# Kernel optimization log

Measured on AMD Instinct MI355X. Metric: run time of the kernel, lower is better.

## Reference

```python
import jax, jax.numpy as jnp
import numpy as np

N_TOKENS = 16384   # flat tokens (e.g., 16 images x 1024 tokens)
E_DIM = 2048       # codebook_dim
N_E = 16384        # codebook_size


def setup_inputs() -> dict:
    key = jax.random.key(0)
    kx, ke = jax.random.split(key)
    x = jax.random.normal(kx, (N_TOKENS, E_DIM), dtype=jnp.float32)
    # nn.Embedding init: uniform(-1/n_e, 1/n_e); scale a normal sample similarly for a realistic magnitude
    embedding = jax.random.uniform(ke, (N_E, E_DIM), dtype=jnp.float32,
                                   minval=-1.0 / N_E, maxval=1.0 / N_E)
    return {"x": x, "embedding": embedding}


def reference(x, embedding):
    # IBQ.quantize, inference path (is_train=False):
    # d[b, n] = ||x_b||^2 + ||e_n||^2 - 2 <x_b, e_n>
    d = (jnp.sum(x * x, axis=1, keepdims=True)
         + jnp.sum(embedding * embedding, axis=1)
         - 2.0 * jnp.einsum('bd,nd->bn', x, embedding))  # [B, n_e]
    min_encoding_indices = jnp.argmin(d, axis=1)          # [B]
    z_q = embedding[min_encoding_indices]                 # [B, e_dim]
    # VQ.forward returns (x, code_idx, codebook_loss=None); loss omitted (non-tensor None)
    return (z_q, min_encoding_indices)
```

## Files before the change

### kernel.cpp

```cpp
#include <hip/hip_runtime.h>
#include <stdint.h>
#include <float.h>

#define K_DIM 2048
#define M_TOK 16384
#define N_EMB 16384
#define NKT 32

typedef int i32x4 __attribute__((ext_vector_type(4)));
typedef unsigned long long u64;
typedef unsigned char u8;

__device__ __forceinline__ uint32_t f2key(float f) {
  uint32_t u = __float_as_uint(f);
  return (u & 0x80000000u) ? ~u : (u | 0x80000000u);
}
__device__ __forceinline__ float key2f(uint32_t k) {
  uint32_t b = (k & 0x80000000u) ? (k & 0x7FFFFFFFu) : ~k;
  return __uint_as_float(b);
}
__device__ __forceinline__ float ulpf(float v) {
  uint32_t e = __float_as_uint(v) & 0x7f800000u;
  return __uint_as_float(e) * 1.1920929e-7f;
}


__global__ void toi8_kernel(const float* __restrict__ in, uint2* __restrict__ out,
                            float scale) {
  long i = (long)blockIdx.x * 256 + threadIdx.x;
  const float4* src = reinterpret_cast<const float4*>(in) + i * 2;
  float4 a = src[0], b = src[1];
  float va[8] = {a.x, a.y, a.z, a.w, b.x, b.y, b.z, b.w};
  uint q[8];
#pragma unroll
  for (int j = 0; j < 8; ++j) {
    int v = (int)rintf(va[j] * scale);
    v = min(127, max(-127, v));
    q[j] = (uint)v & 0xFFu;
  }
  uint2 w;
  w.x = q[0] | (q[1] << 8) | (q[2] << 16) | (q[3] << 24);
  w.y = q[4] | (q[5] << 8) | (q[6] << 16) | (q[7] << 24);
  out[i] = w;
}


__global__ void xx_kernel(const float* __restrict__ x, float* __restrict__ xxArr) {
#pragma clang fp contract(off)
  int row = blockIdx.x * 16 + (threadIdx.x >> 4);
  int blk = threadIdx.x & 15;
  const float* p = x + (long)row * K_DIM + blk * 128;
  float S[16];
#pragma unroll
  for (int L = 0; L < 16; ++L) {
    float p0 = p[L] * p[L];
    float p1 = p[L + 16] * p[L + 16];
    float p2 = p[L + 32] * p[L + 32];
    float p3 = p[L + 48] * p[L + 48];
    float p4 = p[L + 64] * p[L + 64];
    float p5 = p[L + 80] * p[L + 80];
    float p6 = p[L + 96] * p[L + 96];
    float p7 = p[L + 112] * p[L + 112];
    S[L] = ((p0 + p1) + (p2 + p3)) + ((p4 + p5) + (p6 + p7));
  }
  float T1[8], T3[4];
#pragma unroll
  for (int L = 0; L < 8; ++L) T1[L] = S[L] + S[L + 8];
#pragma unroll
  for (int L = 0; L < 4; ++L) T3[L] = T1[L] + T1[L + 4];
  float blksum = (T3[0] + T3[2]) + (T3[1] + T3[3]);
  __shared__ float lds[16][16];
  lds[threadIdx.x >> 4][blk] = blksum;
  __syncthreads();
  if (blk == 0) {
    const float* b = lds[threadIdx.x >> 4];
    float r1[8], r2[4];
#pragma unroll
    for (int i = 0; i < 8; ++i) r1[i] = b[2 * i] + b[2 * i + 1];
#pragma unroll
    for (int i = 0; i < 4; ++i) r2[i] = r1[2 * i] + r1[2 * i + 1];
    xxArr[row] = (r2[0] + r2[1]) + (r2[2] + r2[3]);
  }
}


#define GLOAD_LDS16(g, s)                                              \
  __builtin_amdgcn_global_load_lds(                                    \
      (const __attribute__((address_space(1))) void*)(g),              \
      (__attribute__((address_space(3))) void*)(s), 16, 0, 0)

__global__ __launch_bounds__(512, 2) void gemm_argmin_kernel(
    const u8* __restrict__ x8, const u8* __restrict__ e8,
    u64* __restrict__ stripes) {
  __shared__ __attribute__((aligned(16))) u8 lds[65536];

  int b = blockIdx.x;
  int wg = (b & 7) * 512 + (b >> 3);
  int bx = wg & 63, by = wg >> 6;
  int m0 = by * 256, n0 = bx * 256;

  int t = threadIdx.x;
  int lane = t & 63, wid = t >> 6;
  int wm = wid >> 2, wn = wid & 3;
  int arow = lane & 15, g = lane >> 4;

  int swzb = ((t & 3) ^ ((t >> 3) & 3)) << 4;
  const u8* gA = x8 + (unsigned)(m0 + (t >> 2)) * 2048u + swzb;
  const u8* gB = e8 + (unsigned)(n0 + (t >> 2)) * 2048u + swzb;
  u8* ldst = lds + t * 16;

#define STAGE_H(GSRC, H, KT, BS, LOFF)                                 \
  GLOAD_LDS16((GSRC) + (H) * 262144 + (KT) * 64,                       \
              ldst + (BS) * 32768 + (LOFF) + (H) * 8192)

  i32x4 acc[8][4] = {};
  i32x4 a[4], b0r[2], b1r[2];

  int kc = ((g ^ ((arow >> 1) & 3)) << 4);
  const u8* ldsA = lds + (wm * 128 + arow) * 64 + kc;
  const u8* ldsB = lds + 16384 + (wn * 64 + arow) * 64 + kc;

#define RD_A(QA, BS)                                                   \
  _Pragma("unroll") for (int i4 = 0; i4 < 4; ++i4)                     \
    a[i4] = *(const i32x4*)(ldsA + (BS) * 32768 + ((QA) * 4 + i4) * 1024);
#define RD_B(DST, QB, BS)                                              \
  _Pragma("unroll") for (int j2 = 0; j2 < 2; ++j2)                     \
    DST[j2] = *(const i32x4*)(ldsB + (BS) * 32768 + ((QB) * 2 + j2) * 1024);
#define MFMA_Q(QA, QB, BSRC)                                           \
  __builtin_amdgcn_s_setprio(1);                                       \
  _Pragma("unroll") for (int i4 = 0; i4 < 4; ++i4)                     \
  _Pragma("unroll") for (int j2 = 0; j2 < 2; ++j2)                     \
    acc[(QA) * 4 + i4][(QB) * 2 + j2] = __builtin_amdgcn_mfma_i32_16x16x64_i8( \
        a[i4], BSRC[j2], acc[(QA) * 4 + i4][(QB) * 2 + j2], 0, 0, 0);  \
  __builtin_amdgcn_s_setprio(0);
#define BAR() __builtin_amdgcn_s_barrier()
#define VMC(N) asm volatile("s_waitcnt vmcnt(" #N ")" ::: "memory")

#define TILE_STEADY(KT, BS)                                            \
  RD_A(0, BS); RD_B(b0r, 0, BS);                                       \
  STAGE_H(gA, 1, (KT) + 1, (BS) ^ 1, 0);                               \
  BAR(); MFMA_Q(0, 0, b0r); BAR();                                     \
  RD_B(b1r, 1, BS);                                                    \
  BAR(); MFMA_Q(0, 1, b1r); BAR();                                     \
  RD_A(1, BS);                                                         \
  STAGE_H(gB, 0, (KT) + 2, BS, 16384);                                 \
  BAR(); MFMA_Q(1, 1, b1r); BAR();                                     \
  STAGE_H(gB, 1, (KT) + 2, BS, 16384);                                 \
  STAGE_H(gA, 0, (KT) + 2, BS, 0);                                     \
  VMC(3); BAR(); MFMA_Q(1, 0, b0r); BAR();

  STAGE_H(gA, 0, 0, 0, 0); STAGE_H(gA, 1, 0, 0, 0);
  STAGE_H(gB, 0, 0, 0, 16384); STAGE_H(gB, 1, 0, 0, 16384);
  STAGE_H(gB, 0, 1, 1, 16384); STAGE_H(gB, 1, 1, 1, 16384);
  STAGE_H(gA, 0, 1, 1, 0);
  VMC(3);
  BAR();

#pragma unroll 1
  for (int kt = 0; kt < NKT - 2; kt += 2) {
    TILE_STEADY(kt, 0);
    TILE_STEADY(kt + 1, 1);
  }

  RD_A(0, 0); RD_B(b0r, 0, 0);
  STAGE_H(gA, 1, 31, 1, 0);
  BAR(); MFMA_Q(0, 0, b0r); BAR();
  RD_B(b1r, 1, 0);
  BAR(); MFMA_Q(0, 1, b1r); BAR();
  RD_A(1, 0);
  BAR(); MFMA_Q(1, 1, b1r); BAR();
  VMC(0); BAR(); MFMA_Q(1, 0, b0r); BAR();

  RD_A(0, 1); RD_B(b0r, 0, 1);
  MFMA_Q(0, 0, b0r);
  RD_B(b1r, 1, 1);
  MFMA_Q(0, 1, b1r);
  RD_A(1, 1);
  MFMA_Q(1, 1, b1r);
  MFMA_Q(1, 0, b0r);

  const float kS = -2.0f / (21.0f * 127.0f * 16384.0f);
  int stripe = (bx << 2) + wn;
#pragma unroll
  for (int i = 0; i < 8; ++i) {
#pragma unroll
    for (int r = 0; r < 4; ++r) {
      uint32_t p1 = 0xFFFFFFFFu, p2 = 0xFFFFFFFFu;
#pragma unroll
      for (int j = 0; j < 4; ++j) {
        float sv = (float)acc[i][j][r] * kS;
        uint32_t n = (uint32_t)(n0 + wn * 64 + j * 16 + arow);
        uint32_t pk = ((f2key(sv) >> 14) << 14) | n;
        if (pk < p1) { p2 = p1; p1 = pk; }
        else if (pk < p2) { p2 = pk; }
      }
#pragma unroll
      for (int ms = 1; ms < 16; ms <<= 1) {
        uint32_t q1 = __shfl_xor(p1, ms, 64);
        uint32_t q2 = __shfl_xor(p2, ms, 64);
        uint32_t m1 = min(p1, q1);
        uint32_t m2 = min(max(p1, q1), min(p2, q2));
        p1 = m1; p2 = m2;
      }
      if ((lane & 15) == 0) {
        long gm = m0 + wm * 128 + i * 16 + (lane >> 4) * 4 + r;
        stripes[gm * 256 + stripe] = ((u64)p1 << 32) | p2;
      }
    }
  }
#undef STAGE_H
#undef RD_A
#undef RD_B
#undef MFMA_Q
#undef TILE_STEADY
#undef BAR
#undef VMC
}


__global__ void resolve_kernel(const u64* __restrict__ stripes,
                               const float* __restrict__ x,
                               const float* __restrict__ emb,
                               const float* __restrict__ xxArr,
                               float* __restrict__ outIdxF,
                               int* __restrict__ idxOut) {
#pragma clang fp contract(off)
  int w = threadIdx.x >> 6;
  int row = blockIdx.x * 4 + w;
  int lane = threadIdx.x & 63;
  const u64* sp = stripes + (long)row * 256;

  uint32_t mine[8];
  uint32_t pmin = 0xFFFFFFFFu;
#pragma unroll
  for (int q = 0; q < 4; ++q) {
    u64 v = sp[lane + q * 64];
    mine[2 * q] = (uint32_t)(v >> 32);
    mine[2 * q + 1] = (uint32_t)v;
    pmin = min(pmin, mine[2 * q]);
  }
#pragma unroll
  for (int ms = 1; ms < 64; ms <<= 1) pmin = min(pmin, __shfl_xor(pmin, ms, 64));

  float xxf = xxArr[row];
  float smin_lb = key2f((pmin >> 14) << 14);
  float thr = smin_lb + ulpf(fabsf(xxf) + 0.03f) + 5.0e-4f;
  uint32_t kthr = f2key(thr) >> 14;

  int cnt = 0;
#pragma unroll
  for (int q = 0; q < 8; ++q) cnt += ((mine[q] >> 14) <= kthr) ? 1 : 0;
#pragma unroll
  for (int ms = 1; ms < 64; ms <<= 1) cnt += __shfl_xor(cnt, ms, 64);

  __shared__ int cand[4][32];
  __shared__ int ccount[4];
  bool need = (cnt > 1);
  if (lane == 0) ccount[w] = 0;
  __syncthreads();
  if (need) {
#pragma unroll
    for (int q = 0; q < 8; ++q) {
      if ((mine[q] >> 14) <= kthr) {
        int slot = atomicAdd(&ccount[w], 1);
        if (slot < 32) cand[w][slot] = (int)(mine[q] & 0x3FFFu);
      }
    }
  }
  __syncthreads();

  int winner;
  if (!need) {
    winner = (int)(pmin & 0x3FFFu);
  } else {
    int nc = min(ccount[w], 32);
    float bestd = FLT_MAX;
    int bestn = 0x7fffffff;
    const float* xr = x + (long)row * K_DIM;
    for (int c = 0; c < nc; ++c) {
      int n = cand[w][c];
      const float* er = emb + (long)n * K_DIM;
      double ds = 0.0;
      for (int k = lane; k < K_DIM; k += 64)
        ds += (double)xr[k] * (double)er[k];
#pragma unroll
      for (int ms = 1; ms < 64; ms <<= 1) ds += __shfl_xor(ds, ms, 64);
      float dotf = (float)ds;
      float t2 = 2.0f * dotf;
      float dq = xxf - t2;
      if (dq < bestd || (dq == bestd && n < bestn)) { bestd = dq; bestn = n; }
    }
    winner = bestn;
  }
  if (lane == 0) { outIdxF[row] = (float)winner; idxOut[row] = winner; }
}


__global__ void gather_kernel(const float* __restrict__ emb,
                              const int* __restrict__ idx,
                              float* __restrict__ zq) {
  int row = blockIdx.x, t = threadIdx.x;
  long n = idx[row];
  const float4* s = reinterpret_cast<const float4*>(emb + n * K_DIM);
  float4* d = reinterpret_cast<float4*>(zq + (long)row * K_DIM);
  d[t] = s[t];
  d[t + 256] = s[t + 256];
}


extern "C" void kernel_launch(void* const* d_in, const int* in_sizes, int n_in,
                              void* d_out, int out_size, void* d_ws, size_t ws_size,
                              hipStream_t stream) {
  const float* x = (const float*)d_in[0];
  const float* emb = (const float*)d_in[1];
  float* out = (float*)d_out;

  char* ws = (char*)d_ws;
  u8* x8 = (u8*)ws;
  u64* stripes = (u64*)(ws + 33554432);
  float* xxArr = (float*)(ws + 67108864);
  int* idxbuf = (int*)(ws + 67174400);

  u8* e8 = (u8*)d_out;

  toi8_kernel<<<16384, 256, 0, stream>>>(x, (uint2*)x8, 21.0f);
  toi8_kernel<<<16384, 256, 0, stream>>>(emb, (uint2*)e8, 2080768.0f);
  xx_kernel<<<1024, 256, 0, stream>>>(x, xxArr);
  gemm_argmin_kernel<<<4096, 512, 0, stream>>>(x8, e8, stripes);
  resolve_kernel<<<4096, 256, 0, stream>>>(stripes, x, emb, xxArr, out + 33554432, idxbuf);
  gather_kernel<<<16384, 256, 0, stream>>>(emb, idxbuf, out);
}
```

Baseline: 1.060 ms.

## Restructure int8 GEMM into 16-wave 4-stage LDS pipeline, vectorize resolve dot

The GEMM-argmin kernel goes from 512 threads with a double-buffered 64KB LDS ring to 1024 threads with a 4-stage 128KB ring. Each wave now computes a 64x64 tile instead of 128x64, and the hand-interleaved quarter-tile schedule with many barriers becomes a simple loop with one barrier per k-step and loads issued three steps ahead. The aim is to cut barrier stalls and hide global load latency better. The cost is one block per CU and a tighter per-thread register budget under the new launch bounds, which risks spills. The resolve kernel's candidate dot product also switches to float4 loads.

```diff
diff --git a/kernel.cpp b/kernel.cpp
--- a/kernel.cpp
+++ b/kernel.cpp
@@ -89,10 +89,10 @@
       (const __attribute__((address_space(1))) void*)(g),              \
       (__attribute__((address_space(3))) void*)(s), 16, 0, 0)
 
-__global__ __launch_bounds__(512, 2) void gemm_argmin_kernel(
+__global__ __launch_bounds__(1024, 4) void gemm_argmin_kernel(
     const u8* __restrict__ x8, const u8* __restrict__ e8,
     u64* __restrict__ stripes) {
-  __shared__ __attribute__((aligned(16))) u8 lds[65536];
+  __shared__ __attribute__((aligned(16))) u8 lds[131072];
 
   int b = blockIdx.x;
   int wg = (b & 7) * 512 + (b >> 3);
@@ -109,80 +109,61 @@
   const u8* gB = e8 + (unsigned)(n0 + (t >> 2)) * 2048u + swzb;
   u8* ldst = lds + t * 16;
 
-#define STAGE_H(GSRC, H, KT, BS, LOFF)                                 \
-  GLOAD_LDS16((GSRC) + (H) * 262144 + (KT) * 64,                       \
-              ldst + (BS) * 32768 + (LOFF) + (H) * 8192)
-
-  i32x4 acc[8][4] = {};
-  i32x4 a[4], b0r[2], b1r[2];
+#define STAGE(KT)                                                      \
+  {                                                                    \
+    u8* _d = ldst + ((KT) & 3) * 32768;                                \
+    GLOAD_LDS16(gA + (KT) * 64, _d);                                   \
+    GLOAD_LDS16(gB + (KT) * 64, _d + 16384);                           \
+  }
+
+  i32x4 acc[4][4] = {};
 
   int kc = ((g ^ ((arow >> 1) & 3)) << 4);
-  const u8* ldsA = lds + (wm * 128 + arow) * 64 + kc;
+  const u8* ldsA = lds + (wm * 64 + arow) * 64 + kc;
   const u8* ldsB = lds + 16384 + (wn * 64 + arow) * 64 + kc;
 
-#define RD_A(QA, BS)                                                   \
-  _Pragma("unroll") for (int i4 = 0; i4 < 4; ++i4)                     \
-    a[i4] = *(const i32x4*)(ldsA + (BS) * 32768 + ((QA) * 4 + i4) * 1024);
-#define RD_B(DST, QB, BS)                                              \
-  _Pragma("unroll") for (int j2 = 0; j2 < 2; ++j2)                     \
-    DST[j2] = *(const i32x4*)(ldsB + (BS) * 32768 + ((QB) * 2 + j2) * 1024);
-#define MFMA_Q(QA, QB, BSRC)                                           \
-  __builtin_amdgcn_s_setprio(1);                                       \
-  _Pragma("unroll") for (int i4 = 0; i4 < 4; ++i4)                     \
-  _Pragma("unroll") for (int j2 = 0; j2 < 2; ++j2)                     \
-    acc[(QA) * 4 + i4][(QB) * 2 + j2] = __builtin_amdgcn_mfma_i32_16x16x64_i8( \
-        a[i4], BSRC[j2], acc[(QA) * 4 + i4][(QB) * 2 + j2], 0, 0, 0);  \
-  __builtin_amdgcn_s_setprio(0);
+#define BODY(KT, DO_STAGE, VN)                                         \
+  {                                                                    \
+    const u8* Ab = ldsA + ((KT) & 3) * 32768;                          \
+    const u8* Bb = ldsB + ((KT) & 3) * 32768;                          \
+    i32x4 a[4], bf[4];                                                 \
+    _Pragma("unroll") for (int i4 = 0; i4 < 4; ++i4)                   \
+      a[i4] = *(const i32x4*)(Ab + i4 * 1024);                         \
+    _Pragma("unroll") for (int j4 = 0; j4 < 4; ++j4)                   \
+      bf[j4] = *(const i32x4*)(Bb + j4 * 1024);                        \
+    if (DO_STAGE) STAGE((KT) + 3);                                     \
+    __builtin_amdgcn_s_setprio(1);                                     \
+    _Pragma("unroll") for (int i4 = 0; i4 < 4; ++i4)                   \
+    _Pragma("unroll") for (int j4 = 0; j4 < 4; ++j4)                   \
+      acc[i4][j4] = __builtin_amdgcn_mfma_i32_16x16x64_i8(             \
+          a[i4], bf[j4], acc[i4][j4], 0, 0, 0);                        \
+    __builtin_amdgcn_s_setprio(0);                                     \
+  }
 #define BAR() __builtin_amdgcn_s_barrier()
 #define VMC(N) asm volatile("s_waitcnt vmcnt(" #N ")" ::: "memory")
 
-#define TILE_STEADY(KT, BS)                                            \
-  RD_A(0, BS); RD_B(b0r, 0, BS);                                       \
-  STAGE_H(gA, 1, (KT) + 1, (BS) ^ 1, 0);                               \
-  BAR(); MFMA_Q(0, 0, b0r); BAR();                                     \
-  RD_B(b1r, 1, BS);                                                    \
-  BAR(); MFMA_Q(0, 1, b1r); BAR();                                     \
-  RD_A(1, BS);                                                         \
-  STAGE_H(gB, 0, (KT) + 2, BS, 16384);                                 \
-  BAR(); MFMA_Q(1, 1, b1r); BAR();                                     \
-  STAGE_H(gB, 1, (KT) + 2, BS, 16384);                                 \
-  STAGE_H(gA, 0, (KT) + 2, BS, 0);                                     \
-  VMC(3); BAR(); MFMA_Q(1, 0, b0r); BAR();
-
-  STAGE_H(gA, 0, 0, 0, 0); STAGE_H(gA, 1, 0, 0, 0);
-  STAGE_H(gB, 0, 0, 0, 16384); STAGE_H(gB, 1, 0, 0, 16384);
-  STAGE_H(gB, 0, 1, 1, 16384); STAGE_H(gB, 1, 1, 1, 16384);
-  STAGE_H(gA, 0, 1, 1, 0);
-  VMC(3);
+  STAGE(0); STAGE(1); STAGE(2);
+  VMC(4);
   BAR();
 
 #pragma unroll 1
-  for (int kt = 0; kt < NKT - 2; kt += 2) {
-    TILE_STEADY(kt, 0);
-    TILE_STEADY(kt + 1, 1);
-  }
-
-  RD_A(0, 0); RD_B(b0r, 0, 0);
-  STAGE_H(gA, 1, 31, 1, 0);
-  BAR(); MFMA_Q(0, 0, b0r); BAR();
-  RD_B(b1r, 1, 0);
-  BAR(); MFMA_Q(0, 1, b1r); BAR();
-  RD_A(1, 0);
-  BAR(); MFMA_Q(1, 1, b1r); BAR();
-  VMC(0); BAR(); MFMA_Q(1, 0, b0r); BAR();
-
-  RD_A(0, 1); RD_B(b0r, 0, 1);
-  MFMA_Q(0, 0, b0r);
-  RD_B(b1r, 1, 1);
-  MFMA_Q(0, 1, b1r);
-  RD_A(1, 1);
-  MFMA_Q(1, 1, b1r);
-  MFMA_Q(1, 0, b0r);
+  for (int kt = 0; kt < NKT - 3; ++kt) {
+    BODY(kt, 1, 0);
+    VMC(4);
+    BAR();
+  }
+  BODY(NKT - 3, 0, 0);
+  VMC(2);
+  BAR();
+  BODY(NKT - 2, 0, 0);
+  VMC(0);
+  BAR();
+  BODY(NKT - 1, 0, 0);
 
   const float kS = -2.0f / (21.0f * 127.0f * 16384.0f);
   int stripe = (bx << 2) + wn;
 #pragma unroll
-  for (int i = 0; i < 8; ++i) {
+  for (int i = 0; i < 4; ++i) {
 #pragma unroll
     for (int r = 0; r < 4; ++r) {
       uint32_t p1 = 0xFFFFFFFFu, p2 = 0xFFFFFFFFu;
@@ -203,16 +184,13 @@
         p1 = m1; p2 = m2;
       }
       if ((lane & 15) == 0) {
-        long gm = m0 + wm * 128 + i * 16 + (lane >> 4) * 4 + r;
+        long gm = m0 + wm * 64 + i * 16 + (lane >> 4) * 4 + r;
         stripes[gm * 256 + stripe] = ((u64)p1 << 32) | p2;
       }
     }
   }
-#undef STAGE_H
-#undef RD_A
-#undef RD_B
-#undef MFMA_Q
-#undef TILE_STEADY
+#undef STAGE
+#undef BODY
 #undef BAR
 #undef VMC
 }
@@ -276,13 +254,19 @@
     int nc = min(ccount[w], 32);
     float bestd = FLT_MAX;
     int bestn = 0x7fffffff;
-    const float* xr = x + (long)row * K_DIM;
+    const float4* xr4 = reinterpret_cast<const float4*>(x + (long)row * K_DIM);
     for (int c = 0; c < nc; ++c) {
       int n = cand[w][c];
-      const float* er = emb + (long)n * K_DIM;
+      const float4* er4 = reinterpret_cast<const float4*>(emb + (long)n * K_DIM);
       double ds = 0.0;
-      for (int k = lane; k < K_DIM; k += 64)
-        ds += (double)xr[k] * (double)er[k];
+#pragma unroll
+      for (int it = 0; it < 8; ++it) {
+        int k4 = lane + it * 64;
+        float4 xv = xr4[k4];
+        float4 ev = er4[k4];
+        ds += (double)xv.x * ev.x + (double)xv.y * ev.y +
+              (double)xv.z * ev.z + (double)xv.w * ev.w;
+      }
 #pragma unroll
       for (int ms = 1; ms < 64; ms <<= 1) ds += __shfl_xor(ds, ms, 64);
       float dotf = (float)ds;
@@ -326,7 +310,7 @@
   toi8_kernel<<<16384, 256, 0, stream>>>(x, (uint2*)x8, 21.0f);
   toi8_kernel<<<16384, 256, 0, stream>>>(emb, (uint2*)e8, 2080768.0f);
   xx_kernel<<<1024, 256, 0, stream>>>(x, xxArr);
-  gemm_argmin_kernel<<<4096, 512, 0, stream>>>(x8, e8, stripes);
+  gemm_argmin_kernel<<<4096, 1024, 0, stream>>>(x8, e8, stripes);
   resolve_kernel<<<4096, 256, 0, stream>>>(stripes, x, emb, xxArr, out + 33554432, idxbuf);
   gather_kernel<<<16384, 256, 0, stream>>>(emb, idxbuf, out);
 }
```

Measured after the change: 865.1 us, median of 3. -18.4%, faster.
